# Performance work log

Hardware: AMD Instinct MI355X
Metric: run time of the kernel (lower is better)

## Reference

```python
import jax, jax.numpy as jnp
import numpy as np

E = 8       # num experts
D = 768     # embed_dim
H = 12      # num heads
F = 3072    # expert hidden = 4*D
TOPK = 2


def setup_inputs() -> dict:
    key = jax.random.key(0)
    ks = jax.random.split(key, 8)
    B, S = 4, 1024
    s = lambda d: 1.0 / np.sqrt(d)
    return {
        "x": jax.random.normal(ks[0], (B, S, D), jnp.float32),
        "w_qkv": jax.random.normal(ks[1], (D, 3 * D), jnp.float32) * s(D),
        "b_qkv": jnp.zeros((3 * D,), jnp.float32),
        "w_o": jax.random.normal(ks[2], (D, D), jnp.float32) * s(D),
        "b_o": jnp.zeros((D,), jnp.float32),
        "w_router": jax.random.normal(ks[3], (D, E), jnp.float32) * s(D),
        "w1": jax.random.normal(ks[4], (E, D, F), jnp.float32) * s(D),
        "b1": jnp.zeros((E, F), jnp.float32),
        "w2": jax.random.normal(ks[5], (E, F, D), jnp.float32) * s(F),
        "b2": jnp.zeros((E, D), jnp.float32),
    }


def reference(x, w_qkv, b_qkv, w_o, b_o, w_router, w1, b1, w2, b2):
    B, S, Dm = x.shape
    hd = Dm // H
    # --- multi-head self-attention ---
    qkv = x @ w_qkv + b_qkv                                  # [B,S,3D]
    q, k, v = jnp.split(qkv, 3, axis=-1)
    resh = lambda t: t.reshape(B, S, H, hd).transpose(0, 2, 1, 3)  # [B,H,S,hd]
    q, k, v = resh(q), resh(k), resh(v)
    scores = jnp.einsum('bhqd,bhkd->bhqk', q, k) / np.sqrt(hd).astype(np.float32)
    attn = jax.nn.softmax(scores, axis=-1)
    ctx = jnp.einsum('bhqk,bhkd->bhqd', attn, v)
    ctx = ctx.transpose(0, 2, 1, 3).reshape(B, S, Dm)
    y = ctx @ w_o + b_o                                      # [B,S,D]
    # --- top-k MoE feed-forward ---
    t = y.reshape(B * S, Dm)                                 # [T,D]
    logits = t @ w_router                                    # [T,E]
    probs = jax.nn.softmax(logits, axis=-1)
    topv, topi = jax.lax.top_k(probs, TOPK)                  # [T,K]
    topw = topv / jnp.sum(topv, axis=-1, keepdims=True)      # renormalized gates
    T = t.shape[0]
    wfull = jnp.zeros_like(probs).at[jnp.arange(T)[:, None], topi].set(topw)  # [T,E]
    # dense all-expert compute, weighted combine (faithful to routed math)
    h = jax.nn.gelu(jnp.einsum('td,edf->etf', t, w1) + b1[:, None, :])  # [E,T,F]
    oe = jnp.einsum('etf,efd->etd', h, w2) + b2[:, None, :]              # [E,T,D]
    out = jnp.einsum('te,etd->td', wfull, oe).reshape(B, S, Dm)
    diagnostics = probs  # router probabilities as diagnostics
    return (out, diagnostics)
```

## Files before the change

### kernel.cpp

```cpp
#include <hip/hip_runtime.h>
#include <hip/hip_bf16.h>
#include <cstdint>
#include <cmath>

#define T_TOK 4096
#define DIM   768
#define HEADS 12
#define HD    64
#define NEXP  8
#define FDIM  3072

typedef __attribute__((ext_vector_type(8))) short short8v;
typedef __attribute__((ext_vector_type(4))) float float4v;

__device__ __forceinline__ float gelu_tanh(float x) {
  float u = 0.7978845608028654f * (x + 0.044715f * x * x * x);
  return 0.5f * x * (1.0f + tanhf(u));
}

__device__ __forceinline__ short f2bf(float x) {
  __hip_bfloat16 h = __float2bfloat16(x);
  return *reinterpret_cast<short*>(&h);
}

__device__ __forceinline__ void gld16(void* lds, const void* g) {
  __builtin_amdgcn_global_load_lds(
      (__attribute__((address_space(1))) void*)(uintptr_t)g,
      (__attribute__((address_space(3))) void*)(uint32_t)(uintptr_t)lds,
      16, 0, 0);
}

template<int TBM, int TBN, bool BFOUT>
__global__ __launch_bounds__(256) void gemm_f32(
    const float* __restrict__ A, const float* __restrict__ W,
    const float* __restrict__ bias, float* __restrict__ C,
    short* __restrict__ Cbf, int M, int N, int K)
{
  constexpr int MM = TBM / 16;
  constexpr int MN = TBN / 16;
  constexpr int AL4 = TBM / 64;
  constexpr int BL4 = TBN / 64;
  __shared__ float As[16][TBM + 4];
  __shared__ float Bs[16][TBN + 4];
  const int bm = blockIdx.y * TBM;
  const int bn = blockIdx.x * TBN;
  const int tid = threadIdx.x;
  const int tr = tid >> 4;
  const int tc = tid & 15;

  float acc[MM][MN] = {};

  for (int k0 = 0; k0 < K; k0 += 16) {
    #pragma unroll
    for (int i = 0; i < AL4; i++) {
      int fidx = tid + i * 256;
      int row = fidx >> 2, c4 = fidx & 3;
      float4 v = *(const float4*)&A[(size_t)(bm + row) * K + k0 + c4 * 4];
      As[c4 * 4 + 0][row] = v.x;
      As[c4 * 4 + 1][row] = v.y;
      As[c4 * 4 + 2][row] = v.z;
      As[c4 * 4 + 3][row] = v.w;
    }
    #pragma unroll
    for (int i = 0; i < BL4; i++) {
      int fidx = tid + i * 256;
      int kk = fidx / (TBN / 4), n4 = fidx % (TBN / 4);
      *(float4*)&Bs[kk][n4 * 4] =
          *(const float4*)&W[(size_t)(k0 + kk) * N + bn + n4 * 4];
    }
    __syncthreads();
    #pragma unroll
    for (int kk = 0; kk < 16; kk++) {
      float a[MM], b[MN];
      #pragma unroll
      for (int u4 = 0; u4 < MM / 4; u4++) {
        float4 t = *(const float4*)&As[kk][tr * MM + u4 * 4];
        a[u4*4+0]=t.x; a[u4*4+1]=t.y; a[u4*4+2]=t.z; a[u4*4+3]=t.w;
      }
      #pragma unroll
      for (int v4 = 0; v4 < MN / 4; v4++) {
        float4 t = *(const float4*)&Bs[kk][tc * MN + v4 * 4];
        b[v4*4+0]=t.x; b[v4*4+1]=t.y; b[v4*4+2]=t.z; b[v4*4+3]=t.w;
      }
      #pragma unroll
      for (int u = 0; u < MM; u++)
        #pragma unroll
        for (int v = 0; v < MN; v++)
          acc[u][v] = fmaf(a[u], b[v], acc[u][v]);
    }
    __syncthreads();
  }

  #pragma unroll
  for (int u = 0; u < MM; u++) {
    int row = bm + tr * MM + u;
    #pragma unroll
    for (int v4 = 0; v4 < MN / 4; v4++) {
      int col = bn + tc * MN + v4 * 4;
      float4 o;
      o.x = acc[u][v4*4+0] + bias[col+0];
      o.y = acc[u][v4*4+1] + bias[col+1];
      o.z = acc[u][v4*4+2] + bias[col+2];
      o.w = acc[u][v4*4+3] + bias[col+3];
      *(float4*)&C[(size_t)row * N + col] = o;
      if (BFOUT) {
        short4 s = make_short4(f2bf(o.x), f2bf(o.y), f2bf(o.z), f2bf(o.w));
        *(short4*)&Cbf[(size_t)row * N + col] = s;
      }
    }
  }
}

__global__ __launch_bounds__(256) void transpose_bf16(
    const float* __restrict__ W, short* __restrict__ WT, int K, int N)
{
  __shared__ float t[32][33];
  const size_t mat = (size_t)K * N;
  const float* Wp = W + blockIdx.z * mat;
  short* WTp = WT + blockIdx.z * mat;
  int n0 = blockIdx.x * 32, k0 = blockIdx.y * 32;
  int tx = threadIdx.x, ty = threadIdx.y;
  #pragma unroll
  for (int i = 0; i < 4; i++)
    t[ty + i * 8][tx] = Wp[(size_t)(k0 + ty + i * 8) * N + n0 + tx];
  __syncthreads();
  #pragma unroll
  for (int i = 0; i < 4; i++)
    WTp[(size_t)(n0 + ty + i * 8) * K + k0 + tx] = f2bf(t[tx][ty + i * 8]);
}

template<int MODE>
__global__ __launch_bounds__(256) void moe_mm(
    const short* __restrict__ A, const short* __restrict__ WT,
    const float* __restrict__ bias, void* __restrict__ Cout,
    int N, int K,
    const int* __restrict__ offsets, const int* __restrict__ perm,
    const int* __restrict__ tmap, const int* __restrict__ tilecnt)
{
  const int bx = blockIdx.x;
  if (bx >= tilecnt[0]) return;
  const int info  = tmap[bx];
  const int e     = info >> 16;
  const int start = offsets[e];
  const int M     = offsets[e + 1] - start;
  const int bm    = (info & 0xffff) * 128;
  const int bn    = blockIdx.y * 128;

  __shared__ short As[4][128][8];
  __shared__ short Bs[4][128][8];
  __shared__ int   perm_s[128];

  const int tid  = threadIdx.x;
  const int lane = tid & 63;
  const int wave = tid >> 6;
  const int wm = wave >> 1, wn = wave & 1;
  const int lr = lane & 15;
  const int kb = lane >> 4;

  const short* WTe = WT + (size_t)e * ((size_t)N * K);
  const float* be  = bias + (size_t)e * N;

  if (MODE == 1) {
    if (tid < 128) {
      int rr = bm + tid;
      perm_s[tid] = (rr < M) ? perm[start + rr] : perm[start];
    }
    __syncthreads();
  }

  const short* asrc0;
  const short* asrc1;
  if (MODE == 1) {
    asrc0 = A + (size_t)perm_s[lane] * K + wave * 8;
    asrc1 = A + (size_t)perm_s[64 + lane] * K + wave * 8;
  } else {
    int r0 = bm + lane;      if (r0 >= M) r0 = M - 1;
    int r1 = bm + 64 + lane; if (r1 >= M) r1 = M - 1;
    asrc0 = A + (size_t)(start + r0) * K + wave * 8;
    asrc1 = A + (size_t)(start + r1) * K + wave * 8;
  }
  const short* bsrc0 = WTe + (size_t)(bn + lane) * K + wave * 8;
  const short* bsrc1 = WTe + (size_t)(bn + 64 + lane) * K + wave * 8;
  short* adst0 = &As[wave][0][0];
  short* adst1 = &As[wave][64][0];
  short* bdst0 = &Bs[wave][0][0];
  short* bdst1 = &Bs[wave][64][0];

  float4v acc[4][4] = {};

  for (int k0 = 0; k0 < K; k0 += 32) {
    __syncthreads();
    gld16(adst0, asrc0 + k0);
    gld16(adst1, asrc1 + k0);
    gld16(bdst0, bsrc0 + k0);
    gld16(bdst1, bsrc1 + k0);
    __syncthreads();

    short8v af[4], bfv[4];
    #pragma unroll
    for (int mi = 0; mi < 4; mi++)
      af[mi] = *(const short8v*)&As[kb][wm * 64 + mi * 16 + lr][0];
    #pragma unroll
    for (int ni = 0; ni < 4; ni++)
      bfv[ni] = *(const short8v*)&Bs[kb][wn * 64 + ni * 16 + lr][0];
    #pragma unroll
    for (int mi = 0; mi < 4; mi++)
      #pragma unroll
      for (int ni = 0; ni < 4; ni++)
        acc[mi][ni] = __builtin_amdgcn_mfma_f32_16x16x32_bf16(
            af[mi], bfv[ni], acc[mi][ni], 0, 0, 0);
  }

  #pragma unroll
  for (int ni = 0; ni < 4; ni++) {
    int col = bn + wn * 64 + ni * 16 + lr;
    float b = be[col];
    #pragma unroll
    for (int mi = 0; mi < 4; mi++) {
      int lrow0 = wm * 64 + mi * 16 + kb * 4;
      #pragma unroll
      for (int r = 0; r < 4; r++) {
        int rr = bm + lrow0 + r;
        if (rr < M) {
          if (MODE == 1) {
            short* C = (short*)Cout;
            C[(size_t)(start + rr) * N + col] = f2bf(gelu_tanh(acc[mi][ni][r] + b));
          } else {
            float* C = (float*)Cout;
            C[(size_t)(start + rr) * N + col] = acc[mi][ni][r] + b;
          }
        }
      }
    }
  }
}

__global__ __launch_bounds__(256) void combine_kernel(
    const float* __restrict__ oe, const int* __restrict__ ppos,
    const float* __restrict__ topg, float* __restrict__ out)
{
  int g = blockIdx.x * 256 + threadIdx.x;
  int t = g / 192;
  int c = (g - t * 192) * 4;
  int p0 = ppos[2 * t], p1 = ppos[2 * t + 1];
  float g0 = topg[2 * t], g1 = topg[2 * t + 1];
  float4 a = *(const float4*)&oe[(size_t)p0 * DIM + c];
  float4 b = *(const float4*)&oe[(size_t)p1 * DIM + c];
  float4 o;
  o.x = g0 * a.x + g1 * b.x;
  o.y = g0 * a.y + g1 * b.y;
  o.z = g0 * a.z + g1 * b.z;
  o.w = g0 * a.w + g1 * b.w;
  *(float4*)&out[(size_t)t * DIM + c] = o;
}

__global__ __launch_bounds__(512) void attn_kernel(
    const float* __restrict__ qkv, float* __restrict__ ctx)
{
  const int qt = blockIdx.x;
  const int bh = blockIdx.y;
  const int b = bh / HEADS, h = bh % HEADS;
  const float* base = qkv + (size_t)b * 1024 * (3 * DIM) + h * 64;

  __shared__ float ks[64 * 64];
  __shared__ float vs[64 * 64];
  __shared__ float lred[2][2][32];

  const int tid   = threadIdx.x;
  const int wv    = tid >> 6;
  const int qhalf = wv & 1;
  const int kq    = wv >> 1;
  const int lane  = tid & 63;
  const int grp   = lane >> 2;
  const int sub   = lane & 3;
  const int q0    = qhalf * 32 + grp * 2;
  const int dpart = sub * 16;

  const float qscale = 0.125f * 1.44269504088896f;
  float qA[16], qB[16], accA[16] = {}, accB[16] = {};
  float lA = 0.f, lB = 0.f;

  {
    const float* qpA = base + (size_t)(qt * 64 + q0) * (3 * DIM) + dpart;
    const float* qpB = qpA + 3 * DIM;
    #pragma unroll
    for (int d4 = 0; d4 < 4; d4++) {
      float4 ta = *(const float4*)(qpA + d4 * 4);
      float4 tb = *(const float4*)(qpB + d4 * 4);
      qA[d4*4+0]=ta.x*qscale; qA[d4*4+1]=ta.y*qscale; qA[d4*4+2]=ta.z*qscale; qA[d4*4+3]=ta.w*qscale;
      qB[d4*4+0]=tb.x*qscale; qB[d4*4+1]=tb.y*qscale; qB[d4*4+2]=tb.z*qscale; qB[d4*4+3]=tb.w*qscale;
    }
  }

  for (int kt = 0; kt < 16; kt++) {
    __syncthreads();
    #pragma unroll
    for (int i = 0; i < 2; i++) {
      int idx = tid + i * 512;
      int r = idx >> 4, c4 = idx & 15;
      const float* kp = base + (size_t)(kt * 64 + r) * (3 * DIM) + c4 * 4;
      *(float4*)&ks[r * 64 + c4 * 4] = *(const float4*)(kp + DIM);
      *(float4*)&vs[r * 64 + c4 * 4] = *(const float4*)(kp + 2 * DIM);
    }
    __syncthreads();

    #pragma unroll 2
    for (int jj = 0; jj < 16; jj++) {
      int j = kq * 16 + jj;
      float4 k0v = *(const float4*)&ks[j * 64 + dpart];
      float4 k1v = *(const float4*)&ks[j * 64 + dpart + 4];
      float4 k2v = *(const float4*)&ks[j * 64 + dpart + 8];
      float4 k3v = *(const float4*)&ks[j * 64 + dpart + 12];
      float a0, a1, a2, a3, b0, b1, b2, b3;
      a0  = qA[0]  * k0v.x; a0 = fmaf(qA[1],  k0v.y, a0);
      a0  = fmaf(qA[2],  k0v.z, a0); a0 = fmaf(qA[3],  k0v.w, a0);
      a1  = qA[4]  * k1v.x; a1 = fmaf(qA[5],  k1v.y, a1);
      a1  = fmaf(qA[6],  k1v.z, a1); a1 = fmaf(qA[7],  k1v.w, a1);
      a2  = qA[8]  * k2v.x; a2 = fmaf(qA[9],  k2v.y, a2);
      a2  = fmaf(qA[10], k2v.z, a2); a2 = fmaf(qA[11], k2v.w, a2);
      a3  = qA[12] * k3v.x; a3 = fmaf(qA[13], k3v.y, a3);
      a3  = fmaf(qA[14], k3v.z, a3); a3 = fmaf(qA[15], k3v.w, a3);
      b0  = qB[0]  * k0v.x; b0 = fmaf(qB[1],  k0v.y, b0);
      b0  = fmaf(qB[2],  k0v.z, b0); b0 = fmaf(qB[3],  k0v.w, b0);
      b1  = qB[4]  * k1v.x; b1 = fmaf(qB[5],  k1v.y, b1);
      b1  = fmaf(qB[6],  k1v.z, b1); b1 = fmaf(qB[7],  k1v.w, b1);
      b2  = qB[8]  * k2v.x; b2 = fmaf(qB[9],  k2v.y, b2);
      b2  = fmaf(qB[10], k2v.z, b2); b2 = fmaf(qB[11], k2v.w, b2);
      b3  = qB[12] * k3v.x; b3 = fmaf(qB[13], k3v.y, b3);
      b3  = fmaf(qB[14], k3v.z, b3); b3 = fmaf(qB[15], k3v.w, b3);
      float sA = (a0 + a1) + (a2 + a3);
      float sB = (b0 + b1) + (b2 + b3);
      sA += __shfl_xor(sA, 1);  sB += __shfl_xor(sB, 1);
      sA += __shfl_xor(sA, 2);  sB += __shfl_xor(sB, 2);
      float pA = exp2f(sA);
      float pB = exp2f(sB);
      lA += pA;  lB += pB;
      float4 v0v = *(const float4*)&vs[j * 64 + dpart];
      float4 v1v = *(const float4*)&vs[j * 64 + dpart + 4];
      float4 v2v = *(const float4*)&vs[j * 64 + dpart + 8];
      float4 v3v = *(const float4*)&vs[j * 64 + dpart + 12];
      float vr[16] = {v0v.x,v0v.y,v0v.z,v0v.w, v1v.x,v1v.y,v1v.z,v1v.w,
                      v2v.x,v2v.y,v2v.z,v2v.w, v3v.x,v3v.y,v3v.z,v3v.w};
      #pragma unroll
      for (int d = 0; d < 16; d++) {
        accA[d] = fmaf(pA, vr[d], accA[d]);
        accB[d] = fmaf(pB, vr[d], accB[d]);
      }
    }
  }

  float* regA = ks + qhalf * 2048;
  float* regB = vs + qhalf * 2048;
  const int r0 = (grp * 2) * 64 + dpart;
  const int r1 = r0 + 64;

  __syncthreads();
  if (kq == 2 || kq == 3) {
    float* buf = (kq == 2) ? regA : regB;
    #pragma unroll
    for (int d4 = 0; d4 < 4; d4++) {
      *(float4*)&buf[r0 + d4*4] =
          make_float4(accA[d4*4], accA[d4*4+1], accA[d4*4+2], accA[d4*4+3]);
      *(float4*)&buf[r1 + d4*4] =
          make_float4(accB[d4*4], accB[d4*4+1], accB[d4*4+2], accB[d4*4+3]);
    }
    if (sub == 0) {
      lred[kq - 2][qhalf][grp * 2]     = lA;
      lred[kq - 2][qhalf][grp * 2 + 1] = lB;
    }
  }
  __syncthreads();
  if (kq == 0 || kq == 1) {
    const float* buf = (kq == 0) ? regA : regB;
    #pragma unroll
    for (int d4 = 0; d4 < 4; d4++) {
      float4 a = *(const float4*)&buf[r0 + d4*4];
      float4 c = *(const float4*)&buf[r1 + d4*4];
      accA[d4*4+0] += a.x; accA[d4*4+1] += a.y; accA[d4*4+2] += a.z; accA[d4*4+3] += a.w;
      accB[d4*4+0] += c.x; accB[d4*4+1] += c.y; accB[d4*4+2] += c.z; accB[d4*4+3] += c.w;
    }
    lA += lred[kq][qhalf][grp * 2];
    lB += lred[kq][qhalf][grp * 2 + 1];
  }
  __syncthreads();
  if (kq == 1) {
    #pragma unroll
    for (int d4 = 0; d4 < 4; d4++) {
      *(float4*)&regA[r0 + d4*4] =
          make_float4(accA[d4*4], accA[d4*4+1], accA[d4*4+2], accA[d4*4+3]);
      *(float4*)&regA[r1 + d4*4] =
          make_float4(accB[d4*4], accB[d4*4+1], accB[d4*4+2], accB[d4*4+3]);
    }
    if (sub == 0) {
      lred[0][qhalf][grp * 2]     = lA;
      lred[0][qhalf][grp * 2 + 1] = lB;
    }
  }
  __syncthreads();
  if (kq == 0) {
    #pragma unroll
    for (int d4 = 0; d4 < 4; d4++) {
      float4 a = *(const float4*)&regA[r0 + d4*4];
      float4 c = *(const float4*)&regA[r1 + d4*4];
      accA[d4*4+0] += a.x; accA[d4*4+1] += a.y; accA[d4*4+2] += a.z; accA[d4*4+3] += a.w;
      accB[d4*4+0] += c.x; accB[d4*4+1] += c.y; accB[d4*4+2] += c.z; accB[d4*4+3] += c.w;
    }
    lA += lred[0][qhalf][grp * 2];
    lB += lred[0][qhalf][grp * 2 + 1];
    float invA = 1.f / lA, invB = 1.f / lB;
    float* opA = ctx + ((size_t)b * 1024 + qt * 64 + q0) * DIM + h * 64 + dpart;
    float* opB = opA + DIM;
    #pragma unroll
    for (int d4 = 0; d4 < 4; d4++) {
      float4 oa, ob;
      oa.x = accA[d4*4+0]*invA; oa.y = accA[d4*4+1]*invA;
      oa.z = accA[d4*4+2]*invA; oa.w = accA[d4*4+3]*invA;
      ob.x = accB[d4*4+0]*invB; ob.y = accB[d4*4+1]*invB;
      ob.z = accB[d4*4+2]*invB; ob.w = accB[d4*4+3]*invB;
      *(float4*)(opA + d4 * 4) = oa;
      *(float4*)(opB + d4 * 4) = ob;
    }
  }
}

__global__ __launch_bounds__(256) void router_kernel(
    const float* __restrict__ y, const float* __restrict__ wr,
    float* __restrict__ probs, int* __restrict__ topi,
    float* __restrict__ topg, int* __restrict__ counts)
{
  __shared__ float w[DIM * NEXP];
  const int tid = threadIdx.x;
  for (int i = tid; i < DIM * NEXP; i += 256) w[i] = wr[i];
  __syncthreads();

  const int t = blockIdx.x * 256 + tid;
  const float* yp = y + (size_t)t * DIM;
  float logit[8] = {};
  for (int d = 0; d < DIM; d++) {
    float xv = yp[d];
    #pragma unroll
    for (int e = 0; e < 8; e++) logit[e] = fmaf(xv, w[d * 8 + e], logit[e]);
  }
  float mx = logit[0];
  #pragma unroll
  for (int e = 1; e < 8; e++) mx = fmaxf(mx, logit[e]);
  float p[8], sum = 0.f;
  #pragma unroll
  for (int e = 0; e < 8; e++) { p[e] = __expf(logit[e] - mx); sum += p[e]; }
  float inv = 1.f / sum;
  #pragma unroll
  for (int e = 0; e < 8; e++) { p[e] *= inv; probs[(size_t)t * 8 + e] = p[e]; }

  int i0 = 0;
  #pragma unroll
  for (int e = 1; e < 8; e++) if (p[e] > p[i0]) i0 = e;
  int i1 = (i0 == 0) ? 1 : 0;
  #pragma unroll
  for (int e = 0; e < 8; e++) if (e != i0 && p[e] > p[i1]) i1 = e;
  float g = p[i0] + p[i1];
  topi[2 * t] = i0;  topi[2 * t + 1] = i1;
  topg[2 * t] = p[i0] / g;  topg[2 * t + 1] = p[i1] / g;
  atomicAdd(&counts[i0], 1);
  atomicAdd(&counts[i1], 1);
}

__global__ void init_meta(int* counts) {
  if (threadIdx.x < 8) counts[threadIdx.x] = 0;
}

__global__ void scan_kernel(const int* __restrict__ counts,
                            int* __restrict__ offsets, int* __restrict__ cursors,
                            int* __restrict__ tmap, int* __restrict__ tilecnt) {
  if (threadIdx.x == 0) {
    int s = 0;
    for (int e = 0; e < 8; e++) { offsets[e] = s; cursors[e] = s; s += counts[e]; }
    offsets[8] = s;
    int tu = 0;
    for (int e = 0; e < 8; e++) {
      int m = counts[e];
      for (int t = 0; t * 128 < m; t++) tmap[tu++] = (e << 16) | t;
    }
    tilecnt[0] = tu;
  }
}

__global__ __launch_bounds__(256) void scatter_kernel(
    const int* __restrict__ topi, int* __restrict__ cursors,
    int* __restrict__ perm, int* __restrict__ ppos)
{
  const int t = blockIdx.x * 256 + threadIdx.x;
  #pragma unroll
  for (int s = 0; s < 2; s++) {
    int e = topi[2 * t + s];
    int pos = atomicAdd(&cursors[e], 1);
    perm[pos] = t;
    ppos[2 * t + s] = pos;
  }
}

extern "C" void kernel_launch(void* const* d_in, const int* in_sizes, int n_in,
                              void* d_out, int out_size, void* d_ws, size_t ws_size,
                              hipStream_t stream) {
  const float* x        = (const float*)d_in[0];
  const float* w_qkv    = (const float*)d_in[1];
  const float* b_qkv    = (const float*)d_in[2];
  const float* w_o      = (const float*)d_in[3];
  const float* b_o      = (const float*)d_in[4];
  const float* w_router = (const float*)d_in[5];
  const float* w1       = (const float*)d_in[6];
  const float* b1       = (const float*)d_in[7];
  const float* w2       = (const float*)d_in[8];
  const float* b2       = (const float*)d_in[9];

  float* out   = (float*)d_out;
  float* probs = out + (size_t)T_TOK * DIM;

  char* ws = (char*)d_ws;
  float* qkv  = (float*)ws;
  short* hbuf = (short*)ws;
  short* wT   = (short*)(ws + 50331648);
  float* ctx  = (float*)(ws + 88080384);
  float* oe   = (float*)(ws + 88080384);
  float* y    = (float*)(ws + 100663296);
  short* ybf  = (short*)(ws + 113246208);
  char*  meta = ws + 119537664;
  int*   counts  = (int*)meta;
  int*   cursors = counts + 8;
  int*   offsets = cursors + 8;
  int*   topi    = offsets + 16;
  float* topg    = (float*)(topi + 8192);
  int*   perm    = (int*)(topg + 8192);
  int*   ppos    = perm + 8192;
  int*   tmap    = ppos + 8192;
  int*   tilecnt = tmap + 80;

  init_meta<<<1, 64, 0, stream>>>(counts);

  gemm_f32<128, 64, false><<<dim3((3 * DIM) / 64, T_TOK / 128), 256, 0, stream>>>(
      x, w_qkv, b_qkv, qkv, nullptr, T_TOK, 3 * DIM, DIM);

  attn_kernel<<<dim3(16, 48), 512, 0, stream>>>(qkv, ctx);

  gemm_f32<64, 64, true><<<dim3(DIM / 64, T_TOK / 64), 256, 0, stream>>>(
      ctx, w_o, b_o, y, ybf, T_TOK, DIM, DIM);

  router_kernel<<<16, 256, 0, stream>>>(y, w_router, probs, topi, topg, counts);
  scan_kernel<<<1, 64, 0, stream>>>(counts, offsets, cursors, tmap, tilecnt);
  scatter_kernel<<<16, 256, 0, stream>>>(topi, cursors, perm, ppos);

  transpose_bf16<<<dim3(FDIM / 32, DIM / 32, NEXP), dim3(32, 8), 0, stream>>>(
      w1, wT, DIM, FDIM);
  moe_mm<1><<<dim3(72, FDIM / 128), 256, 0, stream>>>(
      ybf, wT, b1, hbuf, FDIM, DIM, offsets, perm, tmap, tilecnt);

  transpose_bf16<<<dim3(DIM / 32, FDIM / 32, NEXP), dim3(32, 8), 0, stream>>>(
      w2, wT, FDIM, DIM);
  moe_mm<2><<<dim3(72, DIM / 128), 256, 0, stream>>>(
      hbuf, wT, b2, oe, DIM, FDIM, offsets, perm, tmap, tilecnt);

  combine_kernel<<<(T_TOK * DIM / 4) / 256, 256, 0, stream>>>(oe, ppos, topg, out);
}
```

Before: 1.005 ms.

## Restructure attention so each thread owns a full query row, load K/V via LDS-direct

The attention kernel now uses 256 threads per block, with each lane owning one whole query row (64 dims) instead of splitting it across four lanes and two queries. This removes the per-key shuffle reductions but raises register use to 128 floats for q and acc. K/V tiles are now loaded with global_load_lds direct-to-LDS copies instead of going through registers. The trade-off is higher register pressure and broadcast-heavy LDS reads in exchange for fewer cross-lane operations.

```diff
diff --git a/kernel.cpp b/kernel.cpp
--- a/kernel.cpp
+++ b/kernel.cpp
@@ -29,6 +29,12 @@
       (__attribute__((address_space(3))) void*)(uint32_t)(uintptr_t)lds,
       16, 0, 0);
 }
+
+#define FMA4(a, p, v) \
+  (a).x = fmaf(p, (v).x, (a).x); (a).y = fmaf(p, (v).y, (a).y); \
+  (a).z = fmaf(p, (v).z, (a).z); (a).w = fmaf(p, (v).w, (a).w)
+#define ADD4(a, v) \
+  (a).x += (v).x; (a).y += (v).y; (a).z += (v).z; (a).w += (v).w
 
 template<int TBM, int TBN, bool BFOUT>
 __global__ __launch_bounds__(256) void gemm_f32(
@@ -254,7 +260,7 @@
   *(float4*)&out[(size_t)t * DIM + c] = o;
 }
 
-__global__ __launch_bounds__(512) void attn_kernel(
+__global__ __launch_bounds__(256) void attn_kernel(
     const float* __restrict__ qkv, float* __restrict__ ctx)
 {
   const int qt = blockIdx.x;
@@ -264,161 +270,119 @@
 
   __shared__ float ks[64 * 64];
   __shared__ float vs[64 * 64];
-  __shared__ float lred[2][2][32];
-
-  const int tid   = threadIdx.x;
-  const int wv    = tid >> 6;
-  const int qhalf = wv & 1;
-  const int kq    = wv >> 1;
-  const int lane  = tid & 63;
-  const int grp   = lane >> 2;
-  const int sub   = lane & 3;
-  const int q0    = qhalf * 32 + grp * 2;
-  const int dpart = sub * 16;
+  __shared__ float lred[2][64];
+
+  const int tid  = threadIdx.x;
+  const int kq   = tid >> 6;
+  const int lane = tid & 63;
 
   const float qscale = 0.125f * 1.44269504088896f;
-  float qA[16], qB[16], accA[16] = {}, accB[16] = {};
-  float lA = 0.f, lB = 0.f;
+
+  float4 q[16], acc[16];
+  #pragma unroll
+  for (int i = 0; i < 16; i++) acc[i] = make_float4(0.f, 0.f, 0.f, 0.f);
+  float l = 0.f;
 
   {
-    const float* qpA = base + (size_t)(qt * 64 + q0) * (3 * DIM) + dpart;
-    const float* qpB = qpA + 3 * DIM;
-    #pragma unroll
-    for (int d4 = 0; d4 < 4; d4++) {
-      float4 ta = *(const float4*)(qpA + d4 * 4);
-      float4 tb = *(const float4*)(qpB + d4 * 4);
-      qA[d4*4+0]=ta.x*qscale; qA[d4*4+1]=ta.y*qscale; qA[d4*4+2]=ta.z*qscale; qA[d4*4+3]=ta.w*qscale;
-      qB[d4*4+0]=tb.x*qscale; qB[d4*4+1]=tb.y*qscale; qB[d4*4+2]=tb.z*qscale; qB[d4*4+3]=tb.w*qscale;
-    }
-  }
+    const float* qp = base + (size_t)(qt * 64 + lane) * (3 * DIM);
+    #pragma unroll
+    for (int i = 0; i < 16; i++) {
+      float4 t = *(const float4*)(qp + i * 4);
+      q[i] = make_float4(t.x * qscale, t.y * qscale, t.z * qscale, t.w * qscale);
+    }
+  }
+
+  const float4* ks4 = (const float4*)ks;
+  const float4* vs4 = (const float4*)vs;
 
   for (int kt = 0; kt < 16; kt++) {
     __syncthreads();
     #pragma unroll
-    for (int i = 0; i < 2; i++) {
-      int idx = tid + i * 512;
+    for (int i = 0; i < 4; i++) {
+      int idx = tid + i * 256;
       int r = idx >> 4, c4 = idx & 15;
       const float* kp = base + (size_t)(kt * 64 + r) * (3 * DIM) + c4 * 4;
-      *(float4*)&ks[r * 64 + c4 * 4] = *(const float4*)(kp + DIM);
-      *(float4*)&vs[r * 64 + c4 * 4] = *(const float4*)(kp + 2 * DIM);
+      gld16(&ks[idx * 4], kp + DIM);
+      gld16(&vs[idx * 4], kp + 2 * DIM);
     }
     __syncthreads();
 
     #pragma unroll 2
     for (int jj = 0; jj < 16; jj++) {
       int j = kq * 16 + jj;
-      float4 k0v = *(const float4*)&ks[j * 64 + dpart];
-      float4 k1v = *(const float4*)&ks[j * 64 + dpart + 4];
-      float4 k2v = *(const float4*)&ks[j * 64 + dpart + 8];
-      float4 k3v = *(const float4*)&ks[j * 64 + dpart + 12];
-      float a0, a1, a2, a3, b0, b1, b2, b3;
-      a0  = qA[0]  * k0v.x; a0 = fmaf(qA[1],  k0v.y, a0);
-      a0  = fmaf(qA[2],  k0v.z, a0); a0 = fmaf(qA[3],  k0v.w, a0);
-      a1  = qA[4]  * k1v.x; a1 = fmaf(qA[5],  k1v.y, a1);
-      a1  = fmaf(qA[6],  k1v.z, a1); a1 = fmaf(qA[7],  k1v.w, a1);
-      a2  = qA[8]  * k2v.x; a2 = fmaf(qA[9],  k2v.y, a2);
-      a2  = fmaf(qA[10], k2v.z, a2); a2 = fmaf(qA[11], k2v.w, a2);
-      a3  = qA[12] * k3v.x; a3 = fmaf(qA[13], k3v.y, a3);
-      a3  = fmaf(qA[14], k3v.z, a3); a3 = fmaf(qA[15], k3v.w, a3);
-      b0  = qB[0]  * k0v.x; b0 = fmaf(qB[1],  k0v.y, b0);
-      b0  = fmaf(qB[2],  k0v.z, b0); b0 = fmaf(qB[3],  k0v.w, b0);
-      b1  = qB[4]  * k1v.x; b1 = fmaf(qB[5],  k1v.y, b1);
-      b1  = fmaf(qB[6],  k1v.z, b1); b1 = fmaf(qB[7],  k1v.w, b1);
-      b2  = qB[8]  * k2v.x; b2 = fmaf(qB[9],  k2v.y, b2);
-      b2  = fmaf(qB[10], k2v.z, b2); b2 = fmaf(qB[11], k2v.w, b2);
-      b3  = qB[12] * k3v.x; b3 = fmaf(qB[13], k3v.y, b3);
-      b3  = fmaf(qB[14], k3v.z, b3); b3 = fmaf(qB[15], k3v.w, b3);
-      float sA = (a0 + a1) + (a2 + a3);
-      float sB = (b0 + b1) + (b2 + b3);
-      sA += __shfl_xor(sA, 1);  sB += __shfl_xor(sB, 1);
-      sA += __shfl_xor(sA, 2);  sB += __shfl_xor(sB, 2);
-      float pA = exp2f(sA);
-      float pB = exp2f(sB);
-      lA += pA;  lB += pB;
-      float4 v0v = *(const float4*)&vs[j * 64 + dpart];
-      float4 v1v = *(const float4*)&vs[j * 64 + dpart + 4];
-      float4 v2v = *(const float4*)&vs[j * 64 + dpart + 8];
-      float4 v3v = *(const float4*)&vs[j * 64 + dpart + 12];
-      float vr[16] = {v0v.x,v0v.y,v0v.z,v0v.w, v1v.x,v1v.y,v1v.z,v1v.w,
-                      v2v.x,v2v.y,v2v.z,v2v.w, v3v.x,v3v.y,v3v.z,v3v.w};
-      #pragma unroll
-      for (int d = 0; d < 16; d++) {
-        accA[d] = fmaf(pA, vr[d], accA[d]);
-        accB[d] = fmaf(pB, vr[d], accB[d]);
+      float s0 = 0.f, s1 = 0.f, s2 = 0.f, s3 = 0.f;
+      #pragma unroll
+      for (int c = 0; c < 4; c++) {
+        float4 k0 = ks4[j * 16 + c * 4 + 0];
+        float4 k1 = ks4[j * 16 + c * 4 + 1];
+        float4 k2 = ks4[j * 16 + c * 4 + 2];
+        float4 k3 = ks4[j * 16 + c * 4 + 3];
+        s0 = fmaf(q[c*4+0].x, k0.x, s0); s0 = fmaf(q[c*4+0].y, k0.y, s0);
+        s0 = fmaf(q[c*4+0].z, k0.z, s0); s0 = fmaf(q[c*4+0].w, k0.w, s0);
+        s1 = fmaf(q[c*4+1].x, k1.x, s1); s1 = fmaf(q[c*4+1].y, k1.y, s1);
+        s1 = fmaf(q[c*4+1].z, k1.z, s1); s1 = fmaf(q[c*4+1].w, k1.w, s1);
+        s2 = fmaf(q[c*4+2].x, k2.x, s2); s2 = fmaf(q[c*4+2].y, k2.y, s2);
+        s2 = fmaf(q[c*4+2].z, k2.z, s2); s2 = fmaf(q[c*4+2].w, k2.w, s2);
+        s3 = fmaf(q[c*4+3].x, k3.x, s3); s3 = fmaf(q[c*4+3].y, k3.y, s3);
+        s3 = fmaf(q[c*4+3].z, k3.z, s3); s3 = fmaf(q[c*4+3].w, k3.w, s3);
       }
-    }
-  }
-
-  float* regA = ks + qhalf * 2048;
-  float* regB = vs + qhalf * 2048;
-  const int r0 = (grp * 2) * 64 + dpart;
-  const int r1 = r0 + 64;
+      float p = exp2f((s0 + s1) + (s2 + s3));
+      l += p;
+      #pragma unroll
+      for (int c = 0; c < 4; c++) {
+        float4 v0 = vs4[j * 16 + c * 4 + 0];
+        float4 v1 = vs4[j * 16 + c * 4 + 1];
+        float4 v2 = vs4[j * 16 + c * 4 + 2];
+        float4 v3 = vs4[j * 16 + c * 4 + 3];
+        FMA4(acc[c*4+0], p, v0);
+        FMA4(acc[c*4+1], p, v1);
+        FMA4(acc[c*4+2], p, v2);
+        FMA4(acc[c*4+3], p, v3);
+      }
+    }
+  }
+
+  float* myks = ks + lane * 64;
+  float* myvs = vs + lane * 64;
 
   __syncthreads();
   if (kq == 2 || kq == 3) {
-    float* buf = (kq == 2) ? regA : regB;
-    #pragma unroll
-    for (int d4 = 0; d4 < 4; d4++) {
-      *(float4*)&buf[r0 + d4*4] =
-          make_float4(accA[d4*4], accA[d4*4+1], accA[d4*4+2], accA[d4*4+3]);
-      *(float4*)&buf[r1 + d4*4] =
-          make_float4(accB[d4*4], accB[d4*4+1], accB[d4*4+2], accB[d4*4+3]);
-    }
-    if (sub == 0) {
-      lred[kq - 2][qhalf][grp * 2]     = lA;
-      lred[kq - 2][qhalf][grp * 2 + 1] = lB;
-    }
+    float* buf = (kq == 2) ? myks : myvs;
+    #pragma unroll
+    for (int i = 0; i < 16; i++) *(float4*)&buf[i * 4] = acc[i];
+    lred[kq - 2][lane] = l;
   }
   __syncthreads();
   if (kq == 0 || kq == 1) {
-    const float* buf = (kq == 0) ? regA : regB;
-    #pragma unroll
-    for (int d4 = 0; d4 < 4; d4++) {
-      float4 a = *(const float4*)&buf[r0 + d4*4];
-      float4 c = *(const float4*)&buf[r1 + d4*4];
-      accA[d4*4+0] += a.x; accA[d4*4+1] += a.y; accA[d4*4+2] += a.z; accA[d4*4+3] += a.w;
-      accB[d4*4+0] += c.x; accB[d4*4+1] += c.y; accB[d4*4+2] += c.z; accB[d4*4+3] += c.w;
-    }
-    lA += lred[kq][qhalf][grp * 2];
-    lB += lred[kq][qhalf][grp * 2 + 1];
+    const float* buf = (kq == 0) ? myks : myvs;
+    #pragma unroll
+    for (int i = 0; i < 16; i++) {
+      float4 t = *(const float4*)&buf[i * 4];
+      ADD4(acc[i], t);
+    }
+    l += lred[kq][lane];
   }
   __syncthreads();
   if (kq == 1) {
     #pragma unroll
-    for (int d4 = 0; d4 < 4; d4++) {
-      *(float4*)&regA[r0 + d4*4] =
-          make_float4(accA[d4*4], accA[d4*4+1], accA[d4*4+2], accA[d4*4+3]);
-      *(float4*)&regA[r1 + d4*4] =
-          make_float4(accB[d4*4], accB[d4*4+1], accB[d4*4+2], accB[d4*4+3]);
-    }
-    if (sub == 0) {
-      lred[0][qhalf][grp * 2]     = lA;
-      lred[0][qhalf][grp * 2 + 1] = lB;
-    }
+    for (int i = 0; i < 16; i++) *(float4*)&myks[i * 4] = acc[i];
+    lred[0][lane] = l;
   }
   __syncthreads();
   if (kq == 0) {
     #pragma unroll
-    for (int d4 = 0; d4 < 4; d4++) {
-      float4 a = *(const float4*)&regA[r0 + d4*4];
-      float4 c = *(const float4*)&regA[r1 + d4*4];
-      accA[d4*4+0] += a.x; accA[d4*4+1] += a.y; accA[d4*4+2] += a.z; accA[d4*4+3] += a.w;
-      accB[d4*4+0] += c.x; accB[d4*4+1] += c.y; accB[d4*4+2] += c.z; accB[d4*4+3] += c.w;
-    }
-    lA += lred[0][qhalf][grp * 2];
-    lB += lred[0][qhalf][grp * 2 + 1];
-    float invA = 1.f / lA, invB = 1.f / lB;
-    float* opA = ctx + ((size_t)b * 1024 + qt * 64 + q0) * DIM + h * 64 + dpart;
-    float* opB = opA + DIM;
-    #pragma unroll
-    for (int d4 = 0; d4 < 4; d4++) {
-      float4 oa, ob;
-      oa.x = accA[d4*4+0]*invA; oa.y = accA[d4*4+1]*invA;
-      oa.z = accA[d4*4+2]*invA; oa.w = accA[d4*4+3]*invA;
-      ob.x = accB[d4*4+0]*invB; ob.y = accB[d4*4+1]*invB;
-      ob.z = accB[d4*4+2]*invB; ob.w = accB[d4*4+3]*invB;
-      *(float4*)(opA + d4 * 4) = oa;
-      *(float4*)(opB + d4 * 4) = ob;
+    for (int i = 0; i < 16; i++) {
+      float4 t = *(const float4*)&myks[i * 4];
+      ADD4(acc[i], t);
+    }
+    l += lred[0][lane];
+    float inv = 1.f / l;
+    float* op = ctx + ((size_t)b * 1024 + qt * 64 + lane) * DIM + h * 64;
+    #pragma unroll
+    for (int i = 0; i < 16; i++) {
+      float4 o = make_float4(acc[i].x * inv, acc[i].y * inv,
+                             acc[i].z * inv, acc[i].w * inv);
+      *(float4*)(op + i * 4) = o;
     }
   }
 }
@@ -539,7 +503,7 @@
   gemm_f32<128, 64, false><<<dim3((3 * DIM) / 64, T_TOK / 128), 256, 0, stream>>>(
       x, w_qkv, b_qkv, qkv, nullptr, T_TOK, 3 * DIM, DIM);
 
-  attn_kernel<<<dim3(16, 48), 512, 0, stream>>>(qkv, ctx);
+  attn_kernel<<<dim3(16, 48), 256, 0, stream>>>(qkv, ctx);
 
   gemm_f32<64, 64, true><<<dim3(DIM / 64, T_TOK / 64), 256, 0, stream>>>(
       ctx, w_o, b_o, y, ybf, T_TOK, DIM, DIM);
```

Measured after the change: 1.035 ms. +2.9%, slower.
